# Optimization experiments

Measured on AMD Instinct MI355X. Metric: run time of the kernel, lower is better.

Reference implementation:

```python
import jax, jax.numpy as jnp
import numpy as np

B = 8
NUM_HEADS = 32
HEAD_DIM = 128
EMBED = NUM_HEADS * HEAD_DIM  # 4096
MAX_LEN = 4096
CUR_LEN = 4095  # cache position to write the new token
W_SCALE = 0.02


def setup_inputs() -> dict:
    key = jax.random.key(0)
    ks = jax.random.split(key, 8)
    return {
        "x": jax.random.normal(ks[0], (B, EMBED), jnp.float32),
        "k_cache": jax.random.normal(ks[1], (B, NUM_HEADS, MAX_LEN, HEAD_DIM), jnp.float32),
        "v_cache": jax.random.normal(ks[2], (B, NUM_HEADS, MAX_LEN, HEAD_DIM), jnp.float32),
        "Wq": jax.random.normal(ks[3], (EMBED, EMBED), jnp.float32) * W_SCALE,
        "bq": jnp.zeros((EMBED,), jnp.float32),
        "Wk": jax.random.normal(ks[4], (EMBED, EMBED), jnp.float32) * W_SCALE,
        "bk": jnp.zeros((EMBED,), jnp.float32),
        "Wv": jax.random.normal(ks[5], (EMBED, EMBED), jnp.float32) * W_SCALE,
        "bv": jnp.zeros((EMBED,), jnp.float32),
        "Wo": jax.random.normal(ks[6], (EMBED, EMBED), jnp.float32) * W_SCALE,
        "bo": jnp.zeros((EMBED,), jnp.float32),
        "cur_len": CUR_LEN,
    }


def reference(x, k_cache, v_cache, Wq, bq, Wk, bk, Wv, bv, Wo, bo, cur_len):
    bsz = x.shape[0]
    # QKV projections for the single new token; (B, H, 1, D)
    q = (x @ Wq.T + bq).reshape(bsz, NUM_HEADS, 1, HEAD_DIM)
    k = (x @ Wk.T + bk).reshape(bsz, NUM_HEADS, 1, HEAD_DIM)
    v = (x @ Wv.T + bv).reshape(bsz, NUM_HEADS, 1, HEAD_DIM)
    # KVCache.update: write new k/v at cur_len, then attend over first cur_len+1
    k_cache = k_cache.at[:, :, cur_len:cur_len + 1, :].set(k)
    v_cache = v_cache.at[:, :, cur_len:cur_len + 1, :].set(v)
    full_k = k_cache[:, :, :cur_len + 1, :]  # (B, H, S, D)
    full_v = v_cache[:, :, :cur_len + 1, :]
    scale = 1.0 / jnp.sqrt(jnp.float32(HEAD_DIM))
    scores = jnp.einsum('bhqd,bhkd->bhqk', q, full_k) * scale  # (B, H, 1, S)
    probs = jax.nn.softmax(scores, axis=-1)
    attn = jnp.einsum('bhqk,bhkd->bhqd', probs, full_v)  # (B, H, 1, D)
    attn = attn.reshape(bsz, EMBED)
    return attn @ Wo.T + bo
```

## Files before the change

### kernel.cpp

```cpp
#include <hip/hip_runtime.h>

#define EMBED 4096
#define NHEADS 32
#define HDIM 128
#define MAXLEN 4096
#define BATCH 8
#define NSPLIT 16
#define NKVBLK 512

typedef float __attribute__((ext_vector_type(4))) f32x4;

template<int RPW>
__device__ __forceinline__ void gemm8_body(const float* __restrict__ X,
                                           const float* __restrict__ W,
                                           const float* __restrict__ bias,
                                           float* __restrict__ out, int n)
{
    const int lane = threadIdx.x & 63;

    float acc[RPW][8];
    #pragma unroll
    for (int j = 0; j < RPW; ++j)
        #pragma unroll
        for (int m = 0; m < 8; ++m) acc[j][m] = 0.f;

    const float* wb = W + (size_t)n * EMBED;

    #pragma unroll 1
    for (int i = 0; i < 16; ++i) {
        int c = i * 256 + lane * 4;
        f32x4 wv[RPW];
        #pragma unroll
        for (int j = 0; j < RPW; ++j)
            wv[j] = *(const f32x4*)(wb + (size_t)j * EMBED + c);
        #pragma unroll
        for (int m = 0; m < 8; ++m) {
            f32x4 xv = *(const f32x4*)(X + (size_t)m * EMBED + c);
            #pragma unroll
            for (int j = 0; j < RPW; ++j) {
                acc[j][m] += xv.x * wv[j].x + xv.y * wv[j].y
                           + xv.z * wv[j].z + xv.w * wv[j].w;
            }
        }
    }

    #pragma unroll
    for (int j = 0; j < RPW; ++j)
        #pragma unroll
        for (int m = 0; m < 8; ++m) {
            float v = acc[j][m];
            #pragma unroll
            for (int off = 32; off > 0; off >>= 1) v += __shfl_xor(v, off, 64);
            if (lane == 0) out[(size_t)m * EMBED + n + j] = v + bias[n + j];
        }
}

__global__ __launch_bounds__(256)
void qproj_kernel(const float* __restrict__ x,
                  const float* __restrict__ Wq, const float* __restrict__ bq,
                  float* __restrict__ qkvq)
{
    const int w = threadIdx.x >> 6;
    gemm8_body<4>(x, Wq, bq, qkvq, blockIdx.x * 16 + w * 4);
}

__global__ __launch_bounds__(256)
void mid_kernel(const float* __restrict__ x,
                const float* __restrict__ kc, const float* __restrict__ vc,
                const float* __restrict__ Wk, const float* __restrict__ bk,
                const float* __restrict__ Wv, const float* __restrict__ bv,
                const float* __restrict__ qkvq,
                float* __restrict__ qkvk, float* __restrict__ qkvv,
                const int* __restrict__ clp,
                float* __restrict__ part_acc,
                float* __restrict__ part_ms)
{
    const int bid = blockIdx.x;
    const int tid = threadIdx.x, w = tid >> 6, lane = tid & 63;

    if (bid < NKVBLK) {
        int proj = bid >> 8;
        int n0 = (bid & 255) * 16 + w * 4;
        if (proj == 0) gemm8_body<4>(x, Wk, bk, qkvk, n0);
        else           gemm8_body<4>(x, Wv, bv, qkvv, n0);
        return;
    }

    __shared__ float accs[8][HDIM];
    __shared__ float mls[8][2];

    const int cl = *clp;
    const int CH = (cl + NSPLIT - 1) / NSPLIT;

    const int idx = bid - NKVBLK;
    const int bh = idx & 255;
    const int sp = idx >> 8;
    const int b_ = bh >> 5, h = bh & 31;
    const int half = lane >> 5, col4 = lane & 31;
    const int g = w * 2 + half;

    const int tstart = sp * CH;
    const int tend   = min(cl, tstart + CH);

    const float* q = qkvq + (size_t)b_ * EMBED + h * HDIM;
    const float* K = kc + (size_t)bh * MAXLEN * HDIM + col4 * 4;
    const float* V = vc + (size_t)bh * MAXLEN * HDIM + col4 * 4;

    const float scale = 0.08838834764831845f;
    f32x4 qv = *(const f32x4*)(q + col4 * 4);
    qv *= scale;

    float m = -3.0e38f, l = 0.f;
    f32x4 acc = {0.f, 0.f, 0.f, 0.f};

    for (int base = tstart + g; base < tend; base += 32) {
        f32x4 kv[4], vv[4];
        #pragma unroll
        for (int u = 0; u < 4; ++u) {
            int t = base + u * 8;
            if (t < tend) {
                kv[u] = *(const f32x4*)(K + (size_t)t * HDIM);
                vv[u] = *(const f32x4*)(V + (size_t)t * HDIM);
            }
        }
        #pragma unroll
        for (int u = 0; u < 4; ++u) {
            int t = base + u * 8;
            if (t < tend) {
                float s = qv.x * kv[u].x + qv.y * kv[u].y
                        + qv.z * kv[u].z + qv.w * kv[u].w;
                #pragma unroll
                for (int off = 16; off > 0; off >>= 1)
                    s += __shfl_xor(s, off, 64);
                float mn   = fmaxf(m, s);
                float corr = __expf(m - mn);
                float p    = __expf(s - mn);
                l = l * corr + p;
                acc.x = fmaf(acc.x, corr, p * vv[u].x);
                acc.y = fmaf(acc.y, corr, p * vv[u].y);
                acc.z = fmaf(acc.z, corr, p * vv[u].z);
                acc.w = fmaf(acc.w, corr, p * vv[u].w);
                m = mn;
            }
        }
    }

    if (col4 == 0) { mls[g][0] = m; mls[g][1] = l; }
    *(f32x4*)(&accs[g][col4 * 4]) = acc;
    __syncthreads();

    const size_t pidx = (size_t)bh * NSPLIT + sp;
    if (tid < HDIM) {
        float M = mls[0][0];
        #pragma unroll
        for (int i = 1; i < 8; ++i) M = fmaxf(M, mls[i][0]);
        float L = 0.f, o = 0.f;
        #pragma unroll
        for (int i = 0; i < 8; ++i) {
            float wgt = __expf(mls[i][0] - M);
            L += mls[i][1] * wgt;
            o += accs[i][tid] * wgt;
        }
        part_acc[pidx * HDIM + tid] = o;
        if (tid == 0) {
            part_ms[pidx * 2]     = M;
            part_ms[pidx * 2 + 1] = L;
        }
    }
}

__global__ __launch_bounds__(128)
void combine_kernel(const float* __restrict__ qkvq,
                    const float* __restrict__ qkvk, const float* __restrict__ qkvv,
                    const float* __restrict__ part_acc,
                    const float* __restrict__ part_ms,
                    float* __restrict__ attnO)
{
    __shared__ float sred[2];
    const int bh = blockIdx.x;
    const int b_ = bh >> 5, h = bh & 31;
    const int d = threadIdx.x, lane = d & 63, w = d >> 6;

    const float* q    = qkvq + (size_t)b_ * EMBED + h * HDIM;
    const float* knew = qkvk + (size_t)b_ * EMBED + h * HDIM;
    const float* vnew = qkvv + (size_t)b_ * EMBED + h * HDIM;

    float prod = q[d] * knew[d];
    #pragma unroll
    for (int off = 32; off > 0; off >>= 1) prod += __shfl_xor(prod, off, 64);
    if (lane == 0) sred[w] = prod;
    __syncthreads();
    const float s_new = (sred[0] + sred[1]) * 0.08838834764831845f;

    float M = s_new;
    float ms[NSPLIT], ls[NSPLIT];
    #pragma unroll
    for (int sp = 0; sp < NSPLIT; ++sp) {
        ms[sp] = part_ms[((size_t)bh * NSPLIT + sp) * 2];
        ls[sp] = part_ms[((size_t)bh * NSPLIT + sp) * 2 + 1];
        M = fmaxf(M, ms[sp]);
    }
    float wn = __expf(s_new - M);
    float L = wn;
    float o = wn * vnew[d];
    #pragma unroll
    for (int sp = 0; sp < NSPLIT; ++sp) {
        float wgt = __expf(ms[sp] - M);
        L += ls[sp] * wgt;
        o += part_acc[((size_t)bh * NSPLIT + sp) * HDIM + d] * wgt;
    }
    attnO[(size_t)b_ * EMBED + h * HDIM + d] = o / L;
}

__global__ __launch_bounds__(256)
void out_kernel(const float* __restrict__ attnO,
                const float* __restrict__ Wo, const float* __restrict__ bo,
                float* __restrict__ out)
{
    const int w = threadIdx.x >> 6;
    gemm8_body<2>(attnO, Wo, bo, out, blockIdx.x * 8 + w * 2);
}

extern "C" void kernel_launch(void* const* d_in, const int* in_sizes, int n_in,
                              void* d_out, int out_size, void* d_ws, size_t ws_size,
                              hipStream_t stream) {
    const float* x  = (const float*)d_in[0];
    const float* kc = (const float*)d_in[1];
    const float* vc = (const float*)d_in[2];
    const float* Wq = (const float*)d_in[3];
    const float* bq = (const float*)d_in[4];
    const float* Wk = (const float*)d_in[5];
    const float* bk = (const float*)d_in[6];
    const float* Wv = (const float*)d_in[7];
    const float* bv = (const float*)d_in[8];
    const float* Wo = (const float*)d_in[9];
    const float* bo = (const float*)d_in[10];
    const int* clp  = (const int*)d_in[11];

    float* out  = (float*)d_out;
    float* qkvq = (float*)d_ws;
    float* qkvk = qkvq + (size_t)BATCH * EMBED;
    float* qkvv = qkvk + (size_t)BATCH * EMBED;
    float* attnO = qkvv + (size_t)BATCH * EMBED;
    float* part_acc = attnO + (size_t)BATCH * EMBED;
    float* part_ms  = part_acc + (size_t)256 * NSPLIT * HDIM;

    hipLaunchKernelGGL(qproj_kernel, dim3(256), dim3(256), 0, stream,
                       x, Wq, bq, qkvq);
    hipLaunchKernelGGL(mid_kernel, dim3(NKVBLK + 256 * NSPLIT), dim3(256), 0, stream,
                       x, kc, vc, Wk, bk, Wv, bv, qkvq, qkvk, qkvv, clp,
                       part_acc, part_ms);
    hipLaunchKernelGGL(combine_kernel, dim3(256), dim3(128), 0, stream,
                       qkvq, qkvk, qkvv, part_acc, part_ms, attnO);
    hipLaunchKernelGGL(out_kernel, dim3(512), dim3(256), 0, stream,
                       attnO, Wo, bo, out);
}
```

Measured before the change: 282.5 us.

## Fuse Q/K/V projections into one kernel and split attention into its own launch

Computes the Q, K and V projections in a single kernel of 1536 blocks with 2 rows per wave, writing one packed qkv buffer, instead of running the Q projection alone and folding K/V into the attention kernel. The attention-partial kernel now does only attention. Before, the K/V projection ran concurrently with the KV-cache streaming in one launch. Now the projection phase is a single wider launch with more parallelism per block, and the attention phase is cleaner, at the cost of no longer overlapping the K/V projection with cache reads.

```diff
diff --git a/kernel.cpp b/kernel.cpp
--- a/kernel.cpp
+++ b/kernel.cpp
@@ -6,7 +6,6 @@
 #define MAXLEN 4096
 #define BATCH 8
 #define NSPLIT 16
-#define NKVBLK 512
 
 typedef float __attribute__((ext_vector_type(4))) f32x4;
 
@@ -56,53 +55,46 @@
 }
 
 __global__ __launch_bounds__(256)
-void qproj_kernel(const float* __restrict__ x,
-                  const float* __restrict__ Wq, const float* __restrict__ bq,
-                  float* __restrict__ qkvq)
-{
-    const int w = threadIdx.x >> 6;
-    gemm8_body<4>(x, Wq, bq, qkvq, blockIdx.x * 16 + w * 4);
-}
-
-__global__ __launch_bounds__(256)
-void mid_kernel(const float* __restrict__ x,
-                const float* __restrict__ kc, const float* __restrict__ vc,
+void qkv_kernel(const float* __restrict__ x,
+                const float* __restrict__ Wq, const float* __restrict__ bq,
                 const float* __restrict__ Wk, const float* __restrict__ bk,
                 const float* __restrict__ Wv, const float* __restrict__ bv,
-                const float* __restrict__ qkvq,
-                float* __restrict__ qkvk, float* __restrict__ qkvv,
-                const int* __restrict__ clp,
-                float* __restrict__ part_acc,
-                float* __restrict__ part_ms)
-{
-    const int bid = blockIdx.x;
-    const int tid = threadIdx.x, w = tid >> 6, lane = tid & 63;
-
-    if (bid < NKVBLK) {
-        int proj = bid >> 8;
-        int n0 = (bid & 255) * 16 + w * 4;
-        if (proj == 0) gemm8_body<4>(x, Wk, bk, qkvk, n0);
-        else           gemm8_body<4>(x, Wv, bv, qkvv, n0);
-        return;
-    }
-
+                float* __restrict__ qkv )
+{
+    const int w = threadIdx.x >> 6;
+    int ng = blockIdx.x * 8 + w * 2;
+    int proj = ng >> 12;
+    int n = ng & 4095;
+    const float* W = proj == 0 ? Wq : (proj == 1 ? Wk : Wv);
+    const float* b = proj == 0 ? bq : (proj == 1 ? bk : bv);
+    float* out = qkv + (size_t)proj * (BATCH * EMBED);
+    gemm8_body<2>(x, W, b, out, n);
+}
+
+__global__ __launch_bounds__(256)
+void attn_partial(const float* __restrict__ qkv,
+                  const float* __restrict__ kc, const float* __restrict__ vc,
+                  const int* __restrict__ clp,
+                  float* __restrict__ part_acc,
+                  float* __restrict__ part_ms)
+{
     __shared__ float accs[8][HDIM];
     __shared__ float mls[8][2];
 
     const int cl = *clp;
     const int CH = (cl + NSPLIT - 1) / NSPLIT;
 
-    const int idx = bid - NKVBLK;
-    const int bh = idx & 255;
-    const int sp = idx >> 8;
+    const int bh = blockIdx.x & 255;
+    const int sp = blockIdx.x >> 8;
     const int b_ = bh >> 5, h = bh & 31;
+    const int tid = threadIdx.x, w = tid >> 6, lane = tid & 63;
     const int half = lane >> 5, col4 = lane & 31;
     const int g = w * 2 + half;
 
     const int tstart = sp * CH;
     const int tend   = min(cl, tstart + CH);
 
-    const float* q = qkvq + (size_t)b_ * EMBED + h * HDIM;
+    const float* q = qkv + (size_t)b_ * EMBED + h * HDIM;
     const float* K = kc + (size_t)bh * MAXLEN * HDIM + col4 * 4;
     const float* V = vc + (size_t)bh * MAXLEN * HDIM + col4 * 4;
 
@@ -170,8 +162,7 @@
 }
 
 __global__ __launch_bounds__(128)
-void combine_kernel(const float* __restrict__ qkvq,
-                    const float* __restrict__ qkvk, const float* __restrict__ qkvv,
+void combine_kernel(const float* __restrict__ qkv,
                     const float* __restrict__ part_acc,
                     const float* __restrict__ part_ms,
                     float* __restrict__ attnO)
@@ -181,9 +172,9 @@
     const int b_ = bh >> 5, h = bh & 31;
     const int d = threadIdx.x, lane = d & 63, w = d >> 6;
 
-    const float* q    = qkvq + (size_t)b_ * EMBED + h * HDIM;
-    const float* knew = qkvk + (size_t)b_ * EMBED + h * HDIM;
-    const float* vnew = qkvv + (size_t)b_ * EMBED + h * HDIM;
+    const float* q    = qkv + (size_t)b_ * EMBED + h * HDIM;
+    const float* knew = qkv + (size_t)BATCH * EMBED     + (size_t)b_ * EMBED + h * HDIM;
+    const float* vnew = qkv + (size_t)2 * BATCH * EMBED + (size_t)b_ * EMBED + h * HDIM;
 
     float prod = q[d] * knew[d];
     #pragma unroll
@@ -238,20 +229,17 @@
     const int* clp  = (const int*)d_in[11];
 
     float* out  = (float*)d_out;
-    float* qkvq = (float*)d_ws;
-    float* qkvk = qkvq + (size_t)BATCH * EMBED;
-    float* qkvv = qkvk + (size_t)BATCH * EMBED;
-    float* attnO = qkvv + (size_t)BATCH * EMBED;
+    float* qkv  = (float*)d_ws;
+    float* attnO = qkv + (size_t)3 * BATCH * EMBED;
     float* part_acc = attnO + (size_t)BATCH * EMBED;
     float* part_ms  = part_acc + (size_t)256 * NSPLIT * HDIM;
 
-    hipLaunchKernelGGL(qproj_kernel, dim3(256), dim3(256), 0, stream,
-                       x, Wq, bq, qkvq);
-    hipLaunchKernelGGL(mid_kernel, dim3(NKVBLK + 256 * NSPLIT), dim3(256), 0, stream,
-                       x, kc, vc, Wk, bk, Wv, bv, qkvq, qkvk, qkvv, clp,
-                       part_acc, part_ms);
+    hipLaunchKernelGGL(qkv_kernel, dim3(1536), dim3(256), 0, stream,
+                       x, Wq, bq, Wk, bk, Wv, bv, qkv);
+    hipLaunchKernelGGL(attn_partial, dim3(256 * NSPLIT), dim3(256), 0, stream,
+                       qkv, kc, vc, clp, part_acc, part_ms);
     hipLaunchKernelGGL(combine_kernel, dim3(256), dim3(128), 0, stream,
-                       qkvq, qkvk, qkvv, part_acc, part_ms, attnO);
+                       qkv, part_acc, part_ms, attnO);
     hipLaunchKernelGGL(out_kernel, dim3(512), dim3(256), 0, stream,
                        attnO, Wo, bo, out);
 }
```

Measured after the change: 282.1 us. No clear change (-0.2%).
